# Performance work log

Measured on AMD Instinct MI355X. Metric: run time of the kernel, lower is better.

Reference implementation:

```python
import jax, jax.numpy as jnp
import numpy as np

C_IN, C_OUT, K, H, W = 16, 16, 3, 1024, 1024
PAD = 1  # 'same' padding for 3x3 stride-1


def setup_inputs() -> dict:
    key = jax.random.key(0)
    kx, kw, kb = jax.random.split(key, 3)
    x = jax.random.normal(kx, (1, C_IN, H, W), dtype=jnp.float32)
    weight = jax.random.normal(kw, (C_OUT, C_IN, K, K), dtype=jnp.float32) * 0.05
    bias = jax.random.normal(kb, (C_OUT,), dtype=jnp.float32) * 0.05
    return {"x": x, "weight": weight, "bias": bias}


def reference(x, weight, bias):
    # Original module: im2col (unfold) + matmul + reshape + bias add.
    # Mathematically identical to a dense 2D convolution (cross-correlation),
    # expressed here as the fused implicit-GEMM conv primitive.
    out = jax.lax.conv_general_dilated(
        x, weight,
        window_strides=(1, 1),
        padding=((PAD, PAD), (PAD, PAD)),
        dimension_numbers=("NCHW", "OIHW", "NCHW"),
    )  # [1, C_OUT, H, W]
    # out_unf.view(*output_shape) drops the batch dim (batch must be 1)
    return out[0] + bias[:, None, None]
```

## Files before the change

kernel.cpp:

```cpp
#include <hip/hip_runtime.h>


#define HH 1024
#define WW 1024
#define CIN 16
#define HWP (HH * WW)
#define TW 64
#define RPW 4
#define WPB 4
#define HCB 768
#define WLDS 6336

typedef short v8s __attribute__((ext_vector_type(8)));
typedef float v4f __attribute__((ext_vector_type(4)));
typedef unsigned int u32;

__device__ __forceinline__ u32 cvt_pk_bf16(float lo, float hi) {
    u32 r;
    asm("v_cvt_pk_bf16_f32 %0, %1, %2" : "=v"(r) : "v"(lo), "v"(hi));
    return r;
}

__device__ __forceinline__ int swz(int c) { return c ^ ((c >> 3) & 7); }

__global__ __launch_bounds__(256, 3)
void conv3x3_iw(const float* __restrict__ x,
                const float* __restrict__ wgt,
                const float* __restrict__ bias,
                float* __restrict__ out) {
    __shared__ __align__(16) unsigned short sm[WPB * WLDS];

    const int tid = threadIdx.x;
    const int lane = tid & 63;
    const int wave = tid >> 6;
    const int m = lane & 15;
    const int q = lane >> 4;
    const int w0 = blockIdx.x * TW;
    const int y0 = (blockIdx.y * WPB + wave) * RPW;
    unsigned short* smw = sm + wave * WLDS;

    v8s a[5];
    #pragma unroll
    for (int g5 = 0; g5 < 5; ++g5) {
        const int t = 4 * g5 + q;
        union { u32 u[4]; v8s v; } wv;
        if (t < 18) {
            const int base = m * 144 + (t & 1) * 72 + (t >> 1);
            #pragma unroll
            for (int jj = 0; jj < 4; ++jj) {
                const float lo = wgt[base + 18 * jj];
                const float hi = wgt[base + 18 * jj + 9];
                wv.u[jj] = cvt_pk_bf16(lo, hi);
            }
        } else {
            wv.u[0] = wv.u[1] = wv.u[2] = wv.u[3] = 0u;
        }
        a[g5] = wv.v;
    }
    float bl[4];
    #pragma unroll
    for (int i = 0; i < 4; ++i) bl[i] = bias[q * 4 + i];

    int mkw[5], hf5[5], kh5[5];
    #pragma unroll
    for (int g5 = 0; g5 < 5; ++g5) {
        int t = 4 * g5 + q;
        int tt = t > 17 ? 17 : t;
        int khkw = tt >> 1;
        int kh = khkw / 3;
        int kw = khkw - 3 * kh;
        kh5[g5] = kh;
        mkw[g5] = m + kw;
        hf5[g5] = tt & 1;
    }

    auto loadS = [&](int s, float* f) {
        #pragma unroll
        for (int z = 0; z < 2; ++z) {
            const int gh = y0 - 1 + 2 * s + z;
            if ((unsigned)gh < (unsigned)HH) {
                const float* p = x + (size_t)gh * WW + (w0 + lane);
                #pragma unroll
                for (int c = 0; c < CIN; ++c)
                    f[z * 16 + c] = p[(size_t)c * HWP];
            } else {
                #pragma unroll
                for (int c = 0; c < CIN; ++c)
                    f[z * 16 + c] = 0.f;
            }
        }
    };
    auto writeS = [&](int s, const float* f) {
        #pragma unroll
        for (int z = 0; z < 2; ++z) {
            const int slot = 2 * s + z;
            u32 pk[8];
            #pragma unroll
            for (int i = 0; i < 8; ++i)
                pk[i] = cvt_pk_bf16(f[z * 16 + 2 * i], f[z * 16 + 2 * i + 1]);
            const int c0 = slot * 128 + lane * 2;
            *(uint4*)(smw + swz(c0) * 8)     = *(uint4*)&pk[0];
            *(uint4*)(smw + swz(c0 + 1) * 8) = *(uint4*)&pk[4];
        }
    };

    float2 hA, hB;
    auto haloLoad = [&](int j, float2& fp) {
        const int p = lane + 64 * j;
        if (p < 96) {
            const int hp = p >> 3, pc = p & 7;
            const int slot = hp >> 1, side = hp & 1;
            const int gh = y0 - 1 + slot;
            const int gw = side ? (w0 + TW) : (w0 - 1);
            if ((unsigned)gh < (unsigned)HH && (unsigned)gw < (unsigned)WW) {
                const float* p2 = x + (size_t)gh * WW + gw;
                fp.x = p2[(size_t)(2 * pc) * HWP];
                fp.y = p2[(size_t)(2 * pc + 1) * HWP];
            } else {
                fp.x = 0.f; fp.y = 0.f;
            }
        }
    };
    auto haloWrite = [&](int j, float2 fp) {
        const int p = lane + 64 * j;
        if (p < 96) {
            const int hp = p >> 3, pc = p & 7;
            const u32 pk = cvt_pk_bf16(fp.x, fp.y);
            const int ch = HCB + hp * 2 + (pc >> 2);
            *(u32*)(smw + ch * 8 + (pc & 3) * 2) = pk;
        }
    };

    auto computeP = [&](int k) {
        #pragma unroll
        for (int rr = 0; rr < 2; ++rr) {
            const int ib = 2 * k + rr;
            const int R = y0 + ib;
            #pragma unroll
            for (int g16 = 0; g16 < 4; ++g16) {
                v4f acc = {0.f, 0.f, 0.f, 0.f};
                #pragma unroll
                for (int g5 = 0; g5 < 5; ++g5) {
                    const int slot = ib + kh5[g5];
                    const int col = g16 * 16 + mkw[g5] - 1;
                    const int cb = swz(slot * 128 + (col & 63) * 2 + hf5[g5]);
                    const int chl = HCB + slot * 4 + ((col == 64) ? 2 : 0) + hf5[g5];
                    const int c = ((unsigned)col < 64u) ? cb : chl;
                    v8s b = *(const v8s*)(smw + c * 8);
                    acc = __builtin_amdgcn_mfma_f32_16x16x32_bf16(a[g5], b, acc, 0, 0, 0);
                }
                float* op = out + (size_t)R * WW + (w0 + g16 * 16 + m);
                #pragma unroll
                for (int i = 0; i < 4; ++i)
                    op[(size_t)(q * 4 + i) * HWP] = acc[i] + bl[i];
            }
        }
    };

    float A[32], B[32];
    loadS(0, A);
    loadS(1, B);
    haloLoad(0, hA);
    haloLoad(1, hB);
    haloWrite(0, hA);
    haloWrite(1, hB);
    writeS(0, A);
    loadS(2, A);
    writeS(1, B);
    computeP(0);
    writeS(2, A);
    computeP(1);
}

extern "C" void kernel_launch(void* const* d_in, const int* in_sizes, int n_in,
                              void* d_out, int out_size, void* d_ws, size_t ws_size,
                              hipStream_t stream) {
    const float* x = (const float*)d_in[0];
    const float* w = (const float*)d_in[1];
    const float* b = (const float*)d_in[2];
    float* out = (float*)d_out;
    dim3 grid(WW / TW, HH / (RPW * WPB));
    conv3x3_iw<<<grid, dim3(256), 0, stream>>>(x, w, b, out);
}
```

Baseline: 147.6 us.

## Share a 256-wide input tile across the block with vectorized float4 loads

Replaces the per-wave private 64-column tiles with one block-shared LDS tile, 256 columns by 6 input rows, that feeds 4 output rows. All four waves cooperatively fill it using float4 global loads, plus a small halo load, followed by a single block barrier. Each wave then computes its own 64-column slice. The aim is to cut halo overhead and per-load instruction count, and to keep vertically adjacent blocks close in the launch order through the swapped grid. In exchange it drops the earlier staged overlap of loads with MFMA compute and adds a block-wide synchronization.

```diff
diff --git a/kernel.cpp b/kernel.cpp
--- a/kernel.cpp
+++ b/kernel.cpp
@@ -5,11 +5,11 @@
 #define WW 1024
 #define CIN 16
 #define HWP (HH * WW)
-#define TW 64
-#define RPW 4
-#define WPB 4
-#define HCB 768
-#define WLDS 6336
+#define TW 256
+#define TH 4
+#define SLOTS 6
+#define PPS 258
+#define CPS (PPS * 2)
 
 typedef short v8s __attribute__((ext_vector_type(8)));
 typedef float v4f __attribute__((ext_vector_type(4)));
@@ -23,21 +23,28 @@
 
 __device__ __forceinline__ int swz(int c) { return c ^ ((c >> 3) & 7); }
 
+__device__ __forceinline__ void wave_barrier() {
+    __builtin_amdgcn_sched_barrier(0);
+    asm volatile("s_waitcnt lgkmcnt(0)" ::: "memory");
+    __builtin_amdgcn_sched_barrier(0);
+    __builtin_amdgcn_s_barrier();
+    __builtin_amdgcn_sched_barrier(0);
+}
+
 __global__ __launch_bounds__(256, 3)
-void conv3x3_iw(const float* __restrict__ x,
-                const float* __restrict__ wgt,
-                const float* __restrict__ bias,
-                float* __restrict__ out) {
-    __shared__ __align__(16) unsigned short sm[WPB * WLDS];
+void conv3x3_wide(const float* __restrict__ x,
+                  const float* __restrict__ wgt,
+                  const float* __restrict__ bias,
+                  float* __restrict__ out) {
+    __shared__ __align__(16) unsigned short sm[SLOTS * CPS * 8];
 
     const int tid = threadIdx.x;
     const int lane = tid & 63;
     const int wave = tid >> 6;
     const int m = lane & 15;
     const int q = lane >> 4;
-    const int w0 = blockIdx.x * TW;
-    const int y0 = (blockIdx.y * WPB + wave) * RPW;
-    unsigned short* smw = sm + wave * WLDS;
+    const int y0 = blockIdx.x * TH;
+    const int w0 = blockIdx.y * TW;
 
     v8s a[5];
     #pragma unroll
@@ -74,102 +81,100 @@
         hf5[g5] = tt & 1;
     }
 
-    auto loadS = [&](int s, float* f) {
-        #pragma unroll
-        for (int z = 0; z < 2; ++z) {
-            const int gh = y0 - 1 + 2 * s + z;
-            if ((unsigned)gh < (unsigned)HH) {
-                const float* p = x + (size_t)gh * WW + (w0 + lane);
-                #pragma unroll
-                for (int c = 0; c < CIN; ++c)
-                    f[z * 16 + c] = p[(size_t)c * HWP];
-            } else {
-                #pragma unroll
-                for (int c = 0; c < CIN; ++c)
-                    f[z * 16 + c] = 0.f;
-            }
+    auto loadSw = [&](int s0, float4* f8) {
+        const int s = s0 + (tid >> 7);
+        const int gh = y0 - 1 + s;
+        const int c0 = ((tid >> 6) & 1) * 8;
+        if ((unsigned)gh < (unsigned)HH) {
+            const float4* src = (const float4*)(x + (size_t)gh * WW + w0) + lane;
+            #pragma unroll
+            for (int cc = 0; cc < 8; ++cc)
+                f8[cc] = src[(size_t)(c0 + cc) * (HWP / 4)];
+        } else {
+            #pragma unroll
+            for (int cc = 0; cc < 8; ++cc)
+                f8[cc] = make_float4(0.f, 0.f, 0.f, 0.f);
         }
     };
-    auto writeS = [&](int s, const float* f) {
+    auto writeSw = [&](int s0, const float4* f8) {
+        const int s = s0 + (tid >> 7);
+        const int chh = (tid >> 6) & 1;
         #pragma unroll
-        for (int z = 0; z < 2; ++z) {
-            const int slot = 2 * s + z;
-            u32 pk[8];
+        for (int k = 0; k < 4; ++k) {
+            u32 pk[4];
             #pragma unroll
-            for (int i = 0; i < 8; ++i)
-                pk[i] = cvt_pk_bf16(f[z * 16 + 2 * i], f[z * 16 + 2 * i + 1]);
-            const int c0 = slot * 128 + lane * 2;
-            *(uint4*)(smw + swz(c0) * 8)     = *(uint4*)&pk[0];
-            *(uint4*)(smw + swz(c0 + 1) * 8) = *(uint4*)&pk[4];
+            for (int i = 0; i < 4; ++i) {
+                const float lo = ((const float*)&f8[2 * i])[k];
+                const float hi = ((const float*)&f8[2 * i + 1])[k];
+                pk[i] = cvt_pk_bf16(lo, hi);
+            }
+            const int p = 1 + 4 * lane + k;
+            const int c = s * CPS + p * 2 + chh;
+            *(uint4*)(sm + swz(c) * 8) = *(uint4*)pk;
         }
     };
 
-    float2 hA, hB;
-    auto haloLoad = [&](int j, float2& fp) {
-        const int p = lane + 64 * j;
-        if (p < 96) {
-            const int hp = p >> 3, pc = p & 7;
-            const int slot = hp >> 1, side = hp & 1;
-            const int gh = y0 - 1 + slot;
-            const int gw = side ? (w0 + TW) : (w0 - 1);
-            if ((unsigned)gh < (unsigned)HH && (unsigned)gw < (unsigned)WW) {
-                const float* p2 = x + (size_t)gh * WW + gw;
-                fp.x = p2[(size_t)(2 * pc) * HWP];
-                fp.y = p2[(size_t)(2 * pc + 1) * HWP];
-            } else {
-                fp.x = 0.f; fp.y = 0.f;
-            }
+    auto haloLoad = [&](float* f) {
+        const int slot = tid >> 1;
+        const int side = tid & 1;
+        const int gh = y0 - 1 + slot;
+        const int gw = side ? (w0 + TW) : (w0 - 1);
+        if ((unsigned)gh < (unsigned)HH && (unsigned)gw < (unsigned)WW) {
+            const float* p2 = x + (size_t)gh * WW + gw;
+            #pragma unroll
+            for (int c = 0; c < CIN; ++c) f[c] = p2[(size_t)c * HWP];
+        } else {
+            #pragma unroll
+            for (int c = 0; c < CIN; ++c) f[c] = 0.f;
         }
     };
-    auto haloWrite = [&](int j, float2 fp) {
-        const int p = lane + 64 * j;
-        if (p < 96) {
-            const int hp = p >> 3, pc = p & 7;
-            const u32 pk = cvt_pk_bf16(fp.x, fp.y);
-            const int ch = HCB + hp * 2 + (pc >> 2);
-            *(u32*)(smw + ch * 8 + (pc & 3) * 2) = pk;
-        }
+    auto haloWrite = [&](const float* f) {
+        const int slot = tid >> 1;
+        const int side = tid & 1;
+        const int p = side ? (PPS - 1) : 0;
+        u32 pk[8];
+        #pragma unroll
+        for (int i = 0; i < 8; ++i)
+            pk[i] = cvt_pk_bf16(f[2 * i], f[2 * i + 1]);
+        const int c = slot * CPS + p * 2;
+        *(uint4*)(sm + swz(c) * 8)     = *(uint4*)&pk[0];
+        *(uint4*)(sm + swz(c + 1) * 8) = *(uint4*)&pk[4];
     };
 
-    auto computeP = [&](int k) {
+    float fh[16];
+    if (tid < 12) haloLoad(fh);
+    {
+        float4 f8[8];
+        loadSw(0, f8);
+        writeSw(0, f8);
+        loadSw(2, f8);
+        writeSw(2, f8);
+        loadSw(4, f8);
+        writeSw(4, f8);
+    }
+    if (tid < 12) haloWrite(fh);
+
+    wave_barrier();
+
+    const int wco = wave * 128;
+    #pragma unroll
+    for (int r = 0; r < TH; ++r) {
         #pragma unroll
-        for (int rr = 0; rr < 2; ++rr) {
-            const int ib = 2 * k + rr;
-            const int R = y0 + ib;
+        for (int g16 = 0; g16 < 4; ++g16) {
+            v4f acc = {0.f, 0.f, 0.f, 0.f};
             #pragma unroll
-            for (int g16 = 0; g16 < 4; ++g16) {
-                v4f acc = {0.f, 0.f, 0.f, 0.f};
-                #pragma unroll
-                for (int g5 = 0; g5 < 5; ++g5) {
-                    const int slot = ib + kh5[g5];
-                    const int col = g16 * 16 + mkw[g5] - 1;
-                    const int cb = swz(slot * 128 + (col & 63) * 2 + hf5[g5]);
-                    const int chl = HCB + slot * 4 + ((col == 64) ? 2 : 0) + hf5[g5];
-                    const int c = ((unsigned)col < 64u) ? cb : chl;
-                    v8s b = *(const v8s*)(smw + c * 8);
-                    acc = __builtin_amdgcn_mfma_f32_16x16x32_bf16(a[g5], b, acc, 0, 0, 0);
-                }
-                float* op = out + (size_t)R * WW + (w0 + g16 * 16 + m);
-                #pragma unroll
-                for (int i = 0; i < 4; ++i)
-                    op[(size_t)(q * 4 + i) * HWP] = acc[i] + bl[i];
+            for (int g5 = 0; g5 < 5; ++g5) {
+                const int slot = r + kh5[g5];
+                const int c = slot * CPS + wco + g16 * 32 + mkw[g5] * 2 + hf5[g5];
+                v8s b = *(const v8s*)(sm + swz(c) * 8);
+                acc = __builtin_amdgcn_mfma_f32_16x16x32_bf16(a[g5], b, acc, 0, 0, 0);
             }
+            float* op = out + (size_t)(y0 + r) * WW + (w0 + wave * 64 + g16 * 16 + m);
+            #pragma unroll
+            for (int i = 0; i < 4; ++i)
+                op[(size_t)(q * 4 + i) * HWP] = acc[i] + bl[i];
         }
-    };
-
-    float A[32], B[32];
-    loadS(0, A);
-    loadS(1, B);
-    haloLoad(0, hA);
-    haloLoad(1, hB);
-    haloWrite(0, hA);
-    haloWrite(1, hB);
-    writeS(0, A);
-    loadS(2, A);
-    writeS(1, B);
-    computeP(0);
-    writeS(2, A);
-    computeP(1);
+    }
 }
 
 extern "C" void kernel_launch(void* const* d_in, const int* in_sizes, int n_in,
@@ -179,6 +184,6 @@
     const float* w = (const float*)d_in[1];
     const float* b = (const float*)d_in[2];
     float* out = (float*)d_out;
-    dim3 grid(WW / TW, HH / (RPW * WPB));
-    conv3x3_iw<<<grid, dim3(256), 0, stream>>>(x, w, b, out);
+    dim3 grid(HH / TH, WW / TW);
+    conv3x3_wide<<<grid, dim3(256), 0, stream>>>(x, w, b, out);
 }
```

New measurement: 137.0 us. 7.2% less time.
